# Kernel optimization log

Measured on AMD Instinct MI355X. Metric: run time of the kernel, lower is better.

Reference implementation:

```python
import jax, jax.numpy as jnp
import numpy as np

B, WAY, SHOT = 100, 5, 5            # B = way*shot + n_query = 25 + 75
C1, C2, D = 512, 640, 5             # F_L channels, F1 channels, disturb_num
S_L, S1 = 21, 42                    # F_L spatial, F1 spatial (square)
N = C2 * D                          # MLP width = 3200
WEIGHT = 0.5
EPS = 1e-5
GN_GROUPS = 16


def _dwconv1d(x, w):
    # x: (B, C, L), w: (C, 1, 7) depthwise, pad 3, no bias
    return jax.lax.conv_general_dilated(
        x, w, window_strides=(1,), padding=[(3, 3)],
        dimension_numbers=('NCH', 'OIH', 'NCH'),
        feature_group_count=x.shape[1])


def _group_norm(x, gamma, beta):
    # x: (B, C, L); GroupNorm(16, C), eps=1e-5
    b, c, l = x.shape
    xg = x.reshape(b, GN_GROUPS, -1)
    m = xg.mean(-1, keepdims=True)
    v = xg.var(-1, keepdims=True)
    xn = ((xg - m) * jax.lax.rsqrt(v + EPS)).reshape(b, c, l)
    return xn * gamma[None, :, None] + beta[None, :, None]


def setup_inputs() -> dict:
    key = jax.random.key(0)
    ks = jax.random.split(key, 8)
    inp = {
        'F1': jax.random.normal(ks[0], (B, C2, S1, S1), jnp.float32),
        'F_L': jax.random.normal(ks[1], (B, C1, S_L, S_L), jnp.float32),
        # structure_capture: depthwise Conv1d(C1, C1, 7, groups=C1, bias=False) + GroupNorm(16, C1)
        'sc_w': jax.random.normal(ks[2], (C1, 1, 7), jnp.float32) * 0.05,
        'gn_g': jnp.ones((C1,), jnp.float32),
        'gn_b': jnp.zeros((C1,), jnp.float32),
        # mask_branch: Conv2d(C1,16,1)+BN2d(16)+ReLU+Conv2d(16,D,1)
        'mb1_w': jax.random.normal(ks[3], (16, C1), jnp.float32) * 0.02,
        'mb1_b': jnp.zeros((16,), jnp.float32),
        'bn_g': jnp.ones((16,), jnp.float32),
        'bn_b': jnp.zeros((16,), jnp.float32),
        'mb2_w': jax.random.normal(ks[4], (D, 16), jnp.float32) * 0.02,
        'mb2_b': jnp.zeros((D,), jnp.float32),
        # both_mlp1 (resnet=True): BN1d(N) + Linear(N, N) + ELU
        'bn1d_g': jnp.ones((N,), jnp.float32),
        'bn1d_b': jnp.zeros((N,), jnp.float32),
        'lin_w': jax.random.normal(ks[5], (N, N), jnp.float32) * 0.01,
        'lin_b': jnp.zeros((N,), jnp.float32),
        'way': WAY,
        'shot': SHOT,
    }
    return inp


def _forward(F1, F_L, sc_w, gn_g, gn_b, mb1_w, mb1_b, bn_g, bn_b,
             mb2_w, mb2_b, bn1d_g, bn1d_b, lin_w, lin_b, way, shot):
    b = F_L.shape[0]
    # ---- structure_capture ----
    def gate(z):  # z: (B, C1, L)
        return jax.nn.sigmoid(_group_norm(_dwconv1d(z, sc_w), gn_g, gn_b))
    x_h = gate(F_L.mean(axis=3))[:, :, :, None]   # (B,C1,H,1)
    x_w = gate(F_L.mean(axis=2))[:, :, None, :]   # (B,C1,1,W)
    FLs = F_L * x_h * x_w

    # ---- bilinear upsample to F1 spatial (align_corners=False) ----
    s1 = F1.shape[-1]
    hm = jax.image.resize(FLs, (b, FLs.shape[1], s1, s1), method='bilinear')

    # ---- mask_branch (BatchNorm in eval mode: running_mean=0, running_var=1) ----
    h = jnp.einsum('bchw,oc->bohw', hm, mb1_w) + mb1_b[None, :, None, None]
    h = h * (bn_g * jax.lax.rsqrt(jnp.asarray(1.0 + EPS, h.dtype)))[None, :, None, None] \
        + bn_b[None, :, None, None]
    h = jax.nn.relu(h)
    heat = jnp.einsum('bchw,oc->bohw', h, mb2_w) + mb2_b[None, :, None, None]
    mask = jax.nn.sigmoid(heat)                   # (B, D, S1, S1)

    # ---- integration: fused weighted pooling (avoids (B,C2,D,HW) intermediate) ----
    f1 = F1.reshape(b, F1.shape[1], -1)           # (B, C2, HW)
    mk = mask.reshape(b, mask.shape[1], -1)       # (B, D, HW)
    sow = mk.sum(-1) + 1e-5                       # (B, D)
    vec = jnp.einsum('bcp,bdp->bcd', f1, mk) / sow[:, None, :]
    vec = vec.reshape(b, -1)                      # (B, C2*D)

    # ---- both_mlp1 (BN1d eval) + residual mix ----
    inv = jax.lax.rsqrt(jnp.asarray(1.0 + EPS, vec.dtype))
    z = vec * (bn1d_g * inv)[None, :] + bn1d_b[None, :]
    z = jax.nn.elu(z @ lin_w.T + lin_b[None, :])
    out = (1.0 - WEIGHT) * z + WEIGHT * vec

    support = out[:way * shot].reshape(way, shot, -1).mean(1)
    query = out[way * shot:]
    return support, query


def reference(F1, F_L, sc_w, gn_g, gn_b, mb1_w, mb1_b, bn_g, bn_b,
              mb2_w, mb2_b, bn1d_g, bn1d_b, lin_w, lin_b, way, shot):
    return _forward(F1, F_L, sc_w, gn_g, gn_b, mb1_w, mb1_b, bn_g, bn_b,
                    mb2_w, mb2_b, bn1d_g, bn1d_b, lin_w, lin_b, way, shot)
```

## Files before the change

kernel.cpp:

```cpp
#include <hip/hip_runtime.h>
#include <cstddef>

#define TPB 256

__device__ __forceinline__ float sigmoidf_(float x) {
  return 1.0f / (1.0f + __expf(-x));
}

__device__ __forceinline__ void rzmap(int i, int& j0, int& j1, float& w0, float& w1) {
  if (i == 0)            { j0 = 0;  j1 = 0;  w0 = 1.0f;  w1 = 0.0f; }
  else if (i == 41)      { j0 = 20; j1 = 20; w0 = 1.0f;  w1 = 0.0f; }
  else if ((i & 1) == 0) { int k = i >> 1; j0 = k - 1; j1 = k;     w0 = 0.25f; w1 = 0.75f; }
  else                   { int k = i >> 1; j0 = k;     j1 = k + 1; w0 = 0.75f; w1 = 0.25f; }
}

__global__ __launch_bounds__(256) void k1_gate_proj(
    const float* __restrict__ FL, const float* __restrict__ scw,
    const float* __restrict__ gng, const float* __restrict__ gnb,
    const float* __restrict__ mb1w, float* __restrict__ plc) {
  const int g = blockIdx.x, b = blockIdx.y;
  const int tid = threadIdx.x;
  __shared__ __align__(16) float slab[32 * 441];
  __shared__ float rm[672], cm[672], ch[672], cw[672];
  __shared__ float red[16];

  const float* base = FL + ((size_t)b * 512 + g * 32) * 441;
  const float4* b4 = (const float4*)base;
  float4* sl4 = (float4*)slab;
  for (int i = tid; i < 3528; i += TPB) sl4[i] = b4[i];
  __syncthreads();

  for (int idx = tid; idx < 672; idx += TPB) {
    int c = idx / 21, l = idx - c * 21;
    const float* rowp = slab + c * 441 + l * 21;
    float sr = 0.0f;
    #pragma unroll
    for (int w = 0; w < 21; ++w) sr += rowp[w];
    rm[idx] = sr * (1.0f / 21.0f);
    const float* colp = slab + c * 441 + l;
    float sc = 0.0f;
    #pragma unroll
    for (int h = 0; h < 21; ++h) sc += colp[h * 21];
    cm[idx] = sc * (1.0f / 21.0f);
  }
  __syncthreads();

  for (int idx = tid; idx < 672; idx += TPB) {
    int c = idx / 21, l = idx - c * 21;
    const float* w7 = scw + (g * 32 + c) * 7;
    float ah = 0.0f, aw = 0.0f;
    #pragma unroll
    for (int t = 0; t < 7; ++t) {
      int ll = l + t - 3;
      if (ll >= 0 && ll < 21) {
        float wt = w7[t];
        ah += rm[c * 21 + ll] * wt;
        aw += cm[c * 21 + ll] * wt;
      }
    }
    ch[idx] = ah; cw[idx] = aw;
  }
  __syncthreads();

  float s1 = 0.0f, s2 = 0.0f, s3 = 0.0f, s4v = 0.0f;
  for (int idx = tid; idx < 672; idx += TPB) {
    float x = ch[idx], y = cw[idx];
    s1 += x; s2 += x * x; s3 += y; s4v += y * y;
  }
  #pragma unroll
  for (int off = 32; off; off >>= 1) {
    s1 += __shfl_down(s1, off); s2 += __shfl_down(s2, off);
    s3 += __shfl_down(s3, off); s4v += __shfl_down(s4v, off);
  }
  if ((tid & 63) == 0) {
    int wv = tid >> 6;
    red[wv * 4 + 0] = s1; red[wv * 4 + 1] = s2;
    red[wv * 4 + 2] = s3; red[wv * 4 + 3] = s4v;
  }
  __syncthreads();
  const float S1 = red[0] + red[4] + red[8] + red[12];
  const float S2 = red[1] + red[5] + red[9] + red[13];
  const float S3 = red[2] + red[6] + red[10] + red[14];
  const float S4 = red[3] + red[7] + red[11] + red[15];
  const float invn = 1.0f / 672.0f;
  const float mh = S1 * invn, vh = S2 * invn - mh * mh;
  const float mw = S3 * invn, vw = S4 * invn - mw * mw;
  const float ivh = rsqrtf(vh + 1e-5f), ivw = rsqrtf(vw + 1e-5f);

  for (int idx = tid; idx < 672; idx += TPB) {
    int c = idx / 21;
    float gamma = gng[g * 32 + c], beta = gnb[g * 32 + c];
    ch[idx] = sigmoidf_((ch[idx] - mh) * ivh * gamma + beta);
    cw[idx] = sigmoidf_((cw[idx] - mw) * ivw * gamma + beta);
  }
  __syncthreads();

  float* pp = plc + (size_t)b * 16 * 441;
  for (int p = tid; p < 441; p += TPB) {
    int i = p / 21, j = p - i * 21;
    float acc[16];
    #pragma unroll
    for (int o = 0; o < 16; ++o) acc[o] = 0.0f;
    #pragma unroll 4
    for (int c = 0; c < 32; ++c) {
      float v = slab[c * 441 + p] * ch[c * 21 + i] * cw[c * 21 + j];
      const float* wc = mb1w + g * 32 + c;
      #pragma unroll
      for (int o = 0; o < 16; ++o) acc[o] += v * wc[o * 512];
    }
    #pragma unroll
    for (int o = 0; o < 16; ++o) atomicAdd(pp + (size_t)o * 441 + p, acc[o]);
  }
}

__global__ __launch_bounds__(256) void k2_mask(
    const float* __restrict__ plc, const float* __restrict__ mb1b,
    const float* __restrict__ bng, const float* __restrict__ bnb,
    const float* __restrict__ mb2w, const float* __restrict__ mb2b,
    float* __restrict__ mask, float* __restrict__ sow) {
  const int b = blockIdx.x;
  const int p = blockIdx.y * TPB + threadIdx.x;
  float macc[5] = {0, 0, 0, 0, 0};
  if (p < 1764) {
    int y = p / 42, x = p - y * 42;
    int jy0, jy1, jx0, jx1; float wy0, wy1, wx0, wx1;
    rzmap(y, jy0, jy1, wy0, wy1);
    rzmap(x, jx0, jx1, wx0, wx1);
    const float RSQ = rsqrtf(1.0f + 1e-5f);
    const float* pb = plc + (size_t)b * 16 * 441;
    float h[16];
    #pragma unroll
    for (int o = 0; o < 16; ++o) {
      const float* po = pb + o * 441;
      float hm = wy0 * (wx0 * po[jy0 * 21 + jx0] + wx1 * po[jy0 * 21 + jx1]) +
                 wy1 * (wx0 * po[jy1 * 21 + jx0] + wx1 * po[jy1 * 21 + jx1]);
      float t = (hm + mb1b[o]) * (bng[o] * RSQ) + bnb[o];
      h[o] = t > 0.0f ? t : 0.0f;
    }
    #pragma unroll
    for (int d = 0; d < 5; ++d) {
      float acc = mb2b[d];
      #pragma unroll
      for (int o = 0; o < 16; ++o) acc += mb2w[d * 16 + o] * h[o];
      float mv = sigmoidf_(acc);
      mask[((size_t)b * 5 + d) * 1764 + p] = mv;
      macc[d] = mv;
    }
  }
  #pragma unroll
  for (int off = 32; off; off >>= 1) {
    #pragma unroll
    for (int d = 0; d < 5; ++d) macc[d] += __shfl_down(macc[d], off);
  }
  if ((threadIdx.x & 63) == 0) {
    #pragma unroll
    for (int d = 0; d < 5; ++d) atomicAdd(&sow[b * 5 + d], macc[d]);
  }
}

__global__ __launch_bounds__(256) void k3pre(
    const float* __restrict__ b1d, float* __restrict__ vp) {
  int i = blockIdx.x * TPB + threadIdx.x;
  if (i >= 28 * 3200) return;
  int r = i / 3200, k = i - r * 3200;
  vp[(size_t)(100 + r) * 3200 + k] = (r == 0) ? b1d[k] : 0.0f;
}

__global__ __launch_bounds__(256) void k3_vec(
    const float* __restrict__ F1, const float* __restrict__ mask,
    const float* __restrict__ sow, const float* __restrict__ g1d,
    float* __restrict__ vec_pad, float* __restrict__ vec_r) {
  const int ct = blockIdx.x, b = blockIdx.y;
  __shared__ float4 mkv[2205];
  const float4* msrc = (const float4*)(mask + (size_t)b * 8820);
  for (int i = threadIdx.x; i < 2205; i += TPB) mkv[i] = msrc[i];
  __syncthreads();
  const int wv = threadIdx.x >> 6, lane = threadIdx.x & 63;
  const int c0 = ct * 16 + wv * 4;
  const float4* f0 = (const float4*)(F1 + ((size_t)b * 640 + c0) * 1764);
  float a[4][5] = {};
  for (int q = lane; q < 441; q += 64) {
    float4 f[4];
    #pragma unroll
    for (int j = 0; j < 4; ++j) f[j] = f0[(size_t)j * 441 + q];
    #pragma unroll
    for (int d = 0; d < 5; ++d) {
      float4 m = mkv[d * 441 + q];
      #pragma unroll
      for (int j = 0; j < 4; ++j)
        a[j][d] += f[j].x * m.x + f[j].y * m.y + f[j].z * m.z + f[j].w * m.w;
    }
  }
  #pragma unroll
  for (int off = 32; off; off >>= 1) {
    #pragma unroll
    for (int j = 0; j < 4; ++j)
      #pragma unroll
      for (int d = 0; d < 5; ++d)
        a[j][d] += __shfl_down(a[j][d], off);
  }
  if (lane == 0) {
    const float RSQ = rsqrtf(1.0f + 1e-5f);
    #pragma unroll
    for (int j = 0; j < 4; ++j) {
      #pragma unroll
      for (int d = 0; d < 5; ++d) {
        float inv = 1.0f / (sow[b * 5 + d] + 1e-5f);
        float val = a[j][d] * inv;
        int k = (c0 + j) * 5 + d;
        vec_r[(size_t)b * 3200 + k] = val;
        vec_pad[(size_t)b * 3200 + k] = val * (g1d[k] * RSQ);
      }
    }
  }
}

__global__ __launch_bounds__(256) void k4_gemm(
    const float* __restrict__ A, const float* __restrict__ W,
    float* __restrict__ dacc) {
  const int n0 = blockIdx.x * 64, m0 = blockIdx.y * 64, ks = blockIdx.z;
  const int tid = threadIdx.x, tx = tid & 15, ty = tid >> 4;
  __shared__ float4 As[512], Ws[512];
  const int lr = tid >> 3, lq = tid & 7;
  const float4* Ag = (const float4*)(A + (size_t)(m0 + lr) * 3200) + ks * 200 + lq;
  const float4* Wg = (const float4*)(W + (size_t)(n0 + lr) * 3200) + ks * 200 + lq;
  const float4* Ag2 = Ag + 32 * 800;
  const float4* Wg2 = Wg + 32 * 800;
  float acc[4][4] = {};
  for (int kk = 0; kk < 25; ++kk) {
    __syncthreads();
    As[lq * 64 + lr]      = Ag[kk * 8];
    As[lq * 64 + lr + 32] = Ag2[kk * 8];
    Ws[lq * 64 + lr]      = Wg[kk * 8];
    Ws[lq * 64 + lr + 32] = Wg2[kk * 8];
    __syncthreads();
    #pragma unroll
    for (int kq = 0; kq < 8; ++kq) {
      float4 av[4], wv4[4];
      #pragma unroll
      for (int r = 0; r < 4; ++r) av[r] = As[kq * 64 + ty + 16 * r];
      #pragma unroll
      for (int s = 0; s < 4; ++s) wv4[s] = Ws[kq * 64 + tx + 16 * s];
      #pragma unroll
      for (int r = 0; r < 4; ++r)
        #pragma unroll
        for (int s = 0; s < 4; ++s)
          acc[r][s] += av[r].x * wv4[s].x + av[r].y * wv4[s].y +
                       av[r].z * wv4[s].z + av[r].w * wv4[s].w;
    }
  }
  float* dp = dacc + (size_t)ks * 128 * 3200;
  #pragma unroll
  for (int r = 0; r < 4; ++r) {
    int m = m0 + ty + 16 * r;
    #pragma unroll
    for (int s = 0; s < 4; ++s)
      dp[(size_t)m * 3200 + n0 + tx + 16 * s] = acc[r][s];
  }
}

__global__ __launch_bounds__(256) void k4b_epi(
    const float* __restrict__ dacc, const float* __restrict__ linb,
    const float* __restrict__ vec_r, float* __restrict__ sup,
    float* __restrict__ outq) {
  int i = blockIdx.x * TPB + threadIdx.x;
  if (i >= 320000) return;
  int m = i / 3200, n = i - m * 3200;
  const size_t S = (size_t)128 * 3200;
  size_t o = (size_t)m * 3200 + n;
  size_t oc = (size_t)100 * 3200 + n;
  float d  = dacc[o] + dacc[S + o] + dacc[2 * S + o] + dacc[3 * S + o];
  float c0 = dacc[oc] + dacc[S + oc] + dacc[2 * S + oc] + dacc[3 * S + oc];
  float dv = d + c0 + linb[n];
  float z = dv > 0.0f ? dv : expm1f(dv);
  float out = 0.5f * z + 0.5f * vec_r[i];
  if (m < 25) sup[(size_t)m * 3200 + n] = out;
  else outq[(size_t)(m - 20) * 3200 + n] = out;
}

__global__ __launch_bounds__(256) void k5_support(
    const float* __restrict__ sup, float* __restrict__ outp) {
  int idx = blockIdx.x * TPB + threadIdx.x;
  if (idx >= 16000) return;
  int w = idx / 3200, n = idx - w * 3200;
  float s = 0.0f;
  #pragma unroll
  for (int t = 0; t < 5; ++t) s += sup[(size_t)(w * 5 + t) * 3200 + n];
  outp[idx] = s * 0.2f;
}

extern "C" void kernel_launch(void* const* d_in, const int* in_sizes, int n_in,
                              void* d_out, int out_size, void* d_ws, size_t ws_size,
                              hipStream_t stream) {
  const float* F1   = (const float*)d_in[0];
  const float* FL   = (const float*)d_in[1];
  const float* scw  = (const float*)d_in[2];
  const float* gng  = (const float*)d_in[3];
  const float* gnb  = (const float*)d_in[4];
  const float* mb1w = (const float*)d_in[5];
  const float* mb1b = (const float*)d_in[6];
  const float* bng  = (const float*)d_in[7];
  const float* bnb  = (const float*)d_in[8];
  const float* mb2w = (const float*)d_in[9];
  const float* mb2b = (const float*)d_in[10];
  const float* g1d  = (const float*)d_in[11];
  const float* b1d  = (const float*)d_in[12];
  const float* linw = (const float*)d_in[13];
  const float* linb = (const float*)d_in[14];

  float* ws      = (float*)d_ws;
  float* plc     = ws;
  float* sow     = ws + 705600;
  float* mask    = ws + 706112;
  float* vec_pad = ws + 1588112;
  float* vec_r   = ws + 1997712;
  float* dacc    = ws + 2317712;
  float* sup     = ws + 3956112;
  float* out     = (float*)d_out;

  hipMemsetAsync(plc, 0, (size_t)706112 * sizeof(float), stream);
  k3pre<<<dim3(350), TPB, 0, stream>>>(b1d, vec_pad);
  k1_gate_proj<<<dim3(16, 100), TPB, 0, stream>>>(FL, scw, gng, gnb, mb1w, plc);
  k2_mask<<<dim3(100, 7), TPB, 0, stream>>>(plc, mb1b, bng, bnb, mb2w, mb2b, mask, sow);
  k3_vec<<<dim3(40, 100), TPB, 0, stream>>>(F1, mask, sow, g1d, vec_pad, vec_r);
  k4_gemm<<<dim3(50, 2, 4), TPB, 0, stream>>>(vec_pad, linw, dacc);
  k4b_epi<<<dim3(1250), TPB, 0, stream>>>(dacc, linb, vec_r, sup, out);
  k5_support<<<dim3(63), TPB, 0, stream>>>(sup, out);
}
```

Before: 862.6 us.

## Replace atomics with partial-sum reduction, retile GEMM, fuse support mean into epilogue

The gate projection now writes per-group partial sums and a separate kernel reduces them, replacing global atomicAdds and the large memset. The padding pre-kernel is removed, and the GEMM now covers all 128 rows in one 512-thread block with a 10-way split-K, loading the bias row inline. The support mean is folded into the epilogue with atomics, which drops the separate support kernel. k3_vec reads the mask straight from global memory instead of staging it in LDS. Costs are extra memory traffic for the partials and the 10-way dacc, plus atomic accumulation into the output.

```diff
diff --git a/kernel.cpp b/kernel.cpp
--- a/kernel.cpp
+++ b/kernel.cpp
@@ -17,7 +17,7 @@
 __global__ __launch_bounds__(256) void k1_gate_proj(
     const float* __restrict__ FL, const float* __restrict__ scw,
     const float* __restrict__ gng, const float* __restrict__ gnb,
-    const float* __restrict__ mb1w, float* __restrict__ plc) {
+    const float* __restrict__ mb1w, float* __restrict__ plc_part) {
   const int g = blockIdx.x, b = blockIdx.y;
   const int tid = threadIdx.x;
   __shared__ __align__(16) float slab[32 * 441];
@@ -95,7 +95,7 @@
   }
   __syncthreads();
 
-  float* pp = plc + (size_t)b * 16 * 441;
+  float* pp = plc_part + ((size_t)g * 100 + b) * 7056;
   for (int p = tid; p < 441; p += TPB) {
     int i = p / 21, j = p - i * 21;
     float acc[16];
@@ -109,8 +109,18 @@
       for (int o = 0; o < 16; ++o) acc[o] += v * wc[o * 512];
     }
     #pragma unroll
-    for (int o = 0; o < 16; ++o) atomicAdd(pp + (size_t)o * 441 + p, acc[o]);
-  }
+    for (int o = 0; o < 16; ++o) pp[(size_t)o * 441 + p] = acc[o];
+  }
+}
+
+__global__ __launch_bounds__(256) void k1c_red(
+    const float* __restrict__ pp, float* __restrict__ plc) {
+  int i = blockIdx.x * TPB + threadIdx.x;
+  if (i >= 705600) return;
+  float s = 0.0f;
+  #pragma unroll
+  for (int g = 0; g < 16; ++g) s += pp[(size_t)g * 705600 + i];
+  plc[i] = s;
 }
 
 __global__ __launch_bounds__(256) void k2_mask(
@@ -158,26 +168,15 @@
   }
 }
 
-__global__ __launch_bounds__(256) void k3pre(
-    const float* __restrict__ b1d, float* __restrict__ vp) {
-  int i = blockIdx.x * TPB + threadIdx.x;
-  if (i >= 28 * 3200) return;
-  int r = i / 3200, k = i - r * 3200;
-  vp[(size_t)(100 + r) * 3200 + k] = (r == 0) ? b1d[k] : 0.0f;
-}
-
 __global__ __launch_bounds__(256) void k3_vec(
     const float* __restrict__ F1, const float* __restrict__ mask,
     const float* __restrict__ sow, const float* __restrict__ g1d,
     float* __restrict__ vec_pad, float* __restrict__ vec_r) {
   const int ct = blockIdx.x, b = blockIdx.y;
-  __shared__ float4 mkv[2205];
-  const float4* msrc = (const float4*)(mask + (size_t)b * 8820);
-  for (int i = threadIdx.x; i < 2205; i += TPB) mkv[i] = msrc[i];
-  __syncthreads();
   const int wv = threadIdx.x >> 6, lane = threadIdx.x & 63;
   const int c0 = ct * 16 + wv * 4;
   const float4* f0 = (const float4*)(F1 + ((size_t)b * 640 + c0) * 1764);
+  const float4* mk = (const float4*)(mask + (size_t)b * 8820);
   float a[4][5] = {};
   for (int q = lane; q < 441; q += 64) {
     float4 f[4];
@@ -185,7 +184,7 @@
     for (int j = 0; j < 4; ++j) f[j] = f0[(size_t)j * 441 + q];
     #pragma unroll
     for (int d = 0; d < 5; ++d) {
-      float4 m = mkv[d * 441 + q];
+      float4 m = mk[d * 441 + q];
       #pragma unroll
       for (int j = 0; j < 4; ++j)
         a[j][d] += f[j].x * m.x + f[j].y * m.y + f[j].z * m.z + f[j].w * m.w;
@@ -215,44 +214,51 @@
   }
 }
 
-__global__ __launch_bounds__(256) void k4_gemm(
-    const float* __restrict__ A, const float* __restrict__ W,
-    float* __restrict__ dacc) {
-  const int n0 = blockIdx.x * 64, m0 = blockIdx.y * 64, ks = blockIdx.z;
-  const int tid = threadIdx.x, tx = tid & 15, ty = tid >> 4;
-  __shared__ float4 As[512], Ws[512];
+__global__ __launch_bounds__(512) void k4_gemm(
+    const float* __restrict__ A, const float* __restrict__ b1d,
+    const float* __restrict__ W, float* __restrict__ dacc) {
+  const int n0 = blockIdx.x * 64, ks = blockIdx.z;
+  const int tid = threadIdx.x;
+  const int tx = tid & 15, ty = tid >> 4;
   const int lr = tid >> 3, lq = tid & 7;
-  const float4* Ag = (const float4*)(A + (size_t)(m0 + lr) * 3200) + ks * 200 + lq;
-  const float4* Wg = (const float4*)(W + (size_t)(n0 + lr) * 3200) + ks * 200 + lq;
-  const float4* Ag2 = Ag + 32 * 800;
-  const float4* Wg2 = Wg + 32 * 800;
+  __shared__ float4 As[8 * 132];
+  __shared__ float4 Ws[8 * 68];
+  const float4* A4 = (const float4*)A;
+  const float4* B4 = (const float4*)b1d;
+  const float4* W4 = (const float4*)W;
+  const int kbase = ks * 80;
+  const int r1 = lr + 64;
   float acc[4][4] = {};
-  for (int kk = 0; kk < 25; ++kk) {
+  for (int kk = 0; kk < 10; ++kk) {
     __syncthreads();
-    As[lq * 64 + lr]      = Ag[kk * 8];
-    As[lq * 64 + lr + 32] = Ag2[kk * 8];
-    Ws[lq * 64 + lr]      = Wg[kk * 8];
-    Ws[lq * 64 + lr + 32] = Wg2[kk * 8];
+    const int col = kbase + kk * 8 + lq;
+    As[lq * 132 + lr] = A4[(size_t)lr * 800 + col];
+    float4 va1;
+    if (r1 < 100)       va1 = A4[(size_t)r1 * 800 + col];
+    else if (r1 == 100) va1 = B4[col];
+    else                va1 = make_float4(0.f, 0.f, 0.f, 0.f);
+    As[lq * 132 + r1] = va1;
+    Ws[lq * 68 + lr] = W4[(size_t)(n0 + lr) * 800 + col];
     __syncthreads();
     #pragma unroll
     for (int kq = 0; kq < 8; ++kq) {
-      float4 av[4], wv4[4];
-      #pragma unroll
-      for (int r = 0; r < 4; ++r) av[r] = As[kq * 64 + ty + 16 * r];
-      #pragma unroll
-      for (int s = 0; s < 4; ++s) wv4[s] = Ws[kq * 64 + tx + 16 * s];
+      float4 av[4], bv[4];
+      #pragma unroll
+      for (int r = 0; r < 4; ++r) av[r] = As[kq * 132 + ty + 32 * r];
+      #pragma unroll
+      for (int s = 0; s < 4; ++s) bv[s] = Ws[kq * 68 + tx + 16 * s];
       #pragma unroll
       for (int r = 0; r < 4; ++r)
         #pragma unroll
         for (int s = 0; s < 4; ++s)
-          acc[r][s] += av[r].x * wv4[s].x + av[r].y * wv4[s].y +
-                       av[r].z * wv4[s].z + av[r].w * wv4[s].w;
-    }
-  }
-  float* dp = dacc + (size_t)ks * 128 * 3200;
+          acc[r][s] += av[r].x * bv[s].x + av[r].y * bv[s].y +
+                       av[r].z * bv[s].z + av[r].w * bv[s].w;
+    }
+  }
+  float* dp = dacc + (size_t)ks * 409600;
   #pragma unroll
   for (int r = 0; r < 4; ++r) {
-    int m = m0 + ty + 16 * r;
+    const int m = ty + 32 * r;
     #pragma unroll
     for (int s = 0; s < 4; ++s)
       dp[(size_t)m * 3200 + n0 + tx + 16 * s] = acc[r][s];
@@ -261,32 +267,21 @@
 
 __global__ __launch_bounds__(256) void k4b_epi(
     const float* __restrict__ dacc, const float* __restrict__ linb,
-    const float* __restrict__ vec_r, float* __restrict__ sup,
-    float* __restrict__ outq) {
+    const float* __restrict__ vec_r, float* __restrict__ out) {
   int i = blockIdx.x * TPB + threadIdx.x;
   if (i >= 320000) return;
   int m = i / 3200, n = i - m * 3200;
-  const size_t S = (size_t)128 * 3200;
+  const size_t S = 409600;
   size_t o = (size_t)m * 3200 + n;
   size_t oc = (size_t)100 * 3200 + n;
-  float d  = dacc[o] + dacc[S + o] + dacc[2 * S + o] + dacc[3 * S + o];
-  float c0 = dacc[oc] + dacc[S + oc] + dacc[2 * S + oc] + dacc[3 * S + oc];
+  float d = 0.0f, c0 = 0.0f;
+  #pragma unroll
+  for (int t = 0; t < 10; ++t) { d += dacc[t * S + o]; c0 += dacc[t * S + oc]; }
   float dv = d + c0 + linb[n];
   float z = dv > 0.0f ? dv : expm1f(dv);
-  float out = 0.5f * z + 0.5f * vec_r[i];
-  if (m < 25) sup[(size_t)m * 3200 + n] = out;
-  else outq[(size_t)(m - 20) * 3200 + n] = out;
-}
-
-__global__ __launch_bounds__(256) void k5_support(
-    const float* __restrict__ sup, float* __restrict__ outp) {
-  int idx = blockIdx.x * TPB + threadIdx.x;
-  if (idx >= 16000) return;
-  int w = idx / 3200, n = idx - w * 3200;
-  float s = 0.0f;
-  #pragma unroll
-  for (int t = 0; t < 5; ++t) s += sup[(size_t)(w * 5 + t) * 3200 + n];
-  outp[idx] = s * 0.2f;
+  float ov = 0.5f * z + 0.5f * vec_r[i];
+  if (m < 25) atomicAdd(out + (size_t)(m / 5) * 3200 + n, 0.2f * ov);
+  else        out[(size_t)(m - 20) * 3200 + n] = ov;
 }
 
 extern "C" void kernel_launch(void* const* d_in, const int* in_sizes, int n_in,
@@ -308,22 +303,22 @@
   const float* linw = (const float*)d_in[13];
   const float* linb = (const float*)d_in[14];
 
-  float* ws      = (float*)d_ws;
-  float* plc     = ws;
-  float* sow     = ws + 705600;
-  float* mask    = ws + 706112;
-  float* vec_pad = ws + 1588112;
-  float* vec_r   = ws + 1997712;
-  float* dacc    = ws + 2317712;
-  float* sup     = ws + 3956112;
-  float* out     = (float*)d_out;
-
-  hipMemsetAsync(plc, 0, (size_t)706112 * sizeof(float), stream);
-  k3pre<<<dim3(350), TPB, 0, stream>>>(b1d, vec_pad);
-  k1_gate_proj<<<dim3(16, 100), TPB, 0, stream>>>(FL, scw, gng, gnb, mb1w, plc);
+  float* ws       = (float*)d_ws;
+  float* plc      = ws;
+  float* plc_part = ws + 705600;
+  float* sow      = ws + 11995200;
+  float* mask     = ws + 11995712;
+  float* vec_pad  = ws + 12877712;
+  float* vec_r    = ws + 13197712;
+  float* dacc     = ws + 13517712;
+  float* out      = (float*)d_out;
+
+  hipMemsetAsync(sow, 0, 512 * sizeof(float), stream);
+  hipMemsetAsync(out, 0, 16000 * sizeof(float), stream);
+  k1_gate_proj<<<dim3(16, 100), TPB, 0, stream>>>(FL, scw, gng, gnb, mb1w, plc_part);
+  k1c_red<<<dim3(2757), TPB, 0, stream>>>(plc_part, plc);
   k2_mask<<<dim3(100, 7), TPB, 0, stream>>>(plc, mb1b, bng, bnb, mb2w, mb2b, mask, sow);
   k3_vec<<<dim3(40, 100), TPB, 0, stream>>>(F1, mask, sow, g1d, vec_pad, vec_r);
-  k4_gemm<<<dim3(50, 2, 4), TPB, 0, stream>>>(vec_pad, linw, dacc);
-  k4b_epi<<<dim3(1250), TPB, 0, stream>>>(dacc, linb, vec_r, sup, out);
-  k5_support<<<dim3(63), TPB, 0, stream>>>(sup, out);
-}
+  k4_gemm<<<dim3(50, 1, 10), 512, 0, stream>>>(vec_pad, b1d, linw, dacc);
+  k4b_epi<<<dim3(1250), TPB, 0, stream>>>(dacc, linb, vec_r, out);
+}
```

New measurement: 840.9 us. 1.03x faster.
